# Kernel optimization log

Measured on AMD Instinct MI355X. Metric: run time of the kernel, lower is better.

## Reference

```python
import jax, jax.numpy as jnp
import numpy as np

B, C, H, W = 8, 128, 128, 128
HEADS = 4
EPS_LN = 1e-6
EPS_NORM = 1e-12


def layernorm2d(x, w, b):
    # channel-wise LN over axis 1 of (B,C,H,W)
    mean = x.mean(axis=1, keepdims=True)
    var = ((x - mean) ** 2).mean(axis=1, keepdims=True)
    xn = (x - mean) / jnp.sqrt(var + EPS_LN)
    return xn * w[None, :, None, None] + b[None, :, None, None]


def conv1x1(x, w):
    # w: (O, C) pointwise conv, no bias
    return jnp.einsum('bchw,oc->bohw', x, w)


def dwconv3x3(x, w):
    # w: (C, 1, 3, 3) depthwise conv, SAME padding, no bias
    return jax.lax.conv_general_dilated(
        x, w, window_strides=(1, 1), padding='SAME',
        dimension_numbers=('NCHW', 'OIHW', 'NCHW'),
        feature_group_count=x.shape[1])


def l2norm_lastdim(x):
    n = jnp.sqrt(jnp.sum(x * x, axis=-1, keepdims=True))
    return x / jnp.maximum(n, EPS_NORM)


def setup_inputs() -> dict:
    key = jax.random.key(0)
    ks = jax.random.split(key, 12)
    s = 0.05
    return {
        'state': jax.random.normal(ks[0], (B, C, H, W), jnp.float32),
        'dark': jax.random.normal(ks[1], (B, C, H, W), jnp.float32),
        'nq_w': jnp.ones((C,), jnp.float32),
        'nq_b': jnp.zeros((C,), jnp.float32),
        'nkv_w': jnp.ones((C,), jnp.float32),
        'nkv_b': jnp.zeros((C,), jnp.float32),
        'q_pw': jax.random.normal(ks[2], (C, C), jnp.float32) * s,
        'q_dw': jax.random.normal(ks[3], (C, 1, 3, 3), jnp.float32) * s,
        'k_pw': jax.random.normal(ks[4], (C, C), jnp.float32) * s,
        'k_dw': jax.random.normal(ks[5], (C, 1, 3, 3), jnp.float32) * s,
        'v_pw': jax.random.normal(ks[6], (C, C), jnp.float32) * s,
        'v_dw': jax.random.normal(ks[7], (C, 1, 3, 3), jnp.float32) * s,
        'proj_w': jax.random.normal(ks[8], (C, C), jnp.float32) * s,
        'temperature': jnp.ones((HEADS, 1, 1), jnp.float32),
    }


def reference(state, dark, nq_w, nq_b, nkv_w, nkv_b, q_pw, q_dw, k_pw, k_dw,
              v_pw, v_dw, proj_w, temperature):
    b, c, h, w = state.shape
    dc = c // HEADS
    residual = state

    q = dwconv3x3(conv1x1(layernorm2d(state, nq_w, nq_b), q_pw), q_dw)
    k = dwconv3x3(conv1x1(layernorm2d(dark, nkv_w, nkv_b), k_pw), k_dw)
    v = dwconv3x3(conv1x1(dark, v_pw), v_dw)

    q = q.reshape(b, HEADS, dc, h * w)
    k = k.reshape(b, HEADS, dc, h * w)
    v = v.reshape(b, HEADS, dc, h * w)

    q = l2norm_lastdim(q)
    k = l2norm_lastdim(k)

    # channel-wise attention map: (b, heads, dc, dc)
    attn = jnp.einsum('bhcd,bhed->bhce', q, k) * temperature[None]
    attn = jax.nn.softmax(attn, axis=-1)

    out = jnp.einsum('bhce,bhed->bhcd', attn, v).reshape(b, c, h, w)
    return conv1x1(out, proj_w) + residual
```

## Files before the change

### kernel.cpp

```cpp
#include <hip/hip_runtime.h>
#include <hip/hip_bf16.h>
#include <cstdint>

#define BB 8
#define CC 128
#define HH 128
#define WWID 128
#define HW (HH * WWID)
#define NHEADS 4
#define DC (CC / NHEADS)

typedef unsigned short u16x8 __attribute__((ext_vector_type(8)));
typedef unsigned short u16x4 __attribute__((ext_vector_type(4)));
typedef short s16x8 __attribute__((ext_vector_type(8)));
typedef float f32x4 __attribute__((ext_vector_type(4)));

__device__ __forceinline__ float bf2f(unsigned short u) {
  union { unsigned int i; float f; } c;
  c.i = ((unsigned int)u) << 16;
  return c.f;
}
__device__ __forceinline__ unsigned short f2bf(float f) {
  __hip_bfloat16 h = __float2bfloat16(f);
  return *reinterpret_cast<unsigned short*>(&h);
}

__global__ __launch_bounds__(128) void prep_weights_kernel(
    const float* __restrict__ q_pw, const float* __restrict__ k_pw,
    const float* __restrict__ v_pw, const float* __restrict__ proj_w,
    const float* __restrict__ nq_w, const float* __restrict__ nq_b,
    const float* __restrict__ nkv_w, const float* __restrict__ nkv_b,
    unsigned short* __restrict__ Wq, unsigned short* __restrict__ Wkv,
    unsigned short* __restrict__ Wproj, float* __restrict__ S1q,
    float* __restrict__ S2q, float* __restrict__ S1k, float* __restrict__ S2k) {
  int o = threadIdx.x;
  int which = blockIdx.x;
  if (which == 0) {
    float s1 = 0.f, s2 = 0.f;
    for (int c = 0; c < CC; ++c) {
      float w = q_pw[o * CC + c];
      float wl = w * nq_w[c];
      s1 += wl;
      s2 += w * nq_b[c];
      Wq[o * CC + c] = f2bf(wl);
    }
    S1q[o] = s1;
    S2q[o] = s2;
  } else if (which == 1) {
    float s1 = 0.f, s2 = 0.f;
    for (int c = 0; c < CC; ++c) {
      float w = k_pw[o * CC + c];
      float wl = w * nkv_w[c];
      s1 += wl;
      s2 += w * nkv_b[c];
      Wkv[o * CC + c] = f2bf(wl);
    }
    S1k[o] = s1;
    S2k[o] = s2;
  } else if (which == 2) {
    for (int c = 0; c < CC; ++c) Wkv[(128 + o) * CC + c] = f2bf(v_pw[o * CC + c]);
  } else {
    for (int c = 0; c < CC; ++c) Wproj[o * CC + c] = f2bf(proj_w[o * CC + c]);
  }
}

template <int MT, int LN_ROWS, int IN_BF16, int OUT_F32, int DO_RES>
__global__ __launch_bounds__(256) void conv_mfma_kernel(
    const void* __restrict__ Xv, const unsigned short* __restrict__ Wbf,
    const float* __restrict__ S1, const float* __restrict__ S2,
    const float* __restrict__ res, unsigned short* __restrict__ Out0,
    unsigned short* __restrict__ Out1, float* __restrict__ OutF) {
  constexpr int MPW = MT / 4;
  __shared__ unsigned short Xs[64 * 128];
  __shared__ float sstat[2][4][64];

  int tid = threadIdx.x;
  int lane = tid & 63, wid = tid >> 6;
  int p = tid & 63, qd = tid >> 6;
  int b = blockIdx.y;
  int p0 = blockIdx.x * 64;

  size_t xpix = (size_t)b * CC * HW + p0 + p;
  float s = 0.f, ss = 0.f;
#pragma unroll
  for (int chunk = 0; chunk < 4; ++chunk) {
    u16x8 vals;
#pragma unroll
    for (int j = 0; j < 8; ++j) {
      int c = chunk * 32 + qd * 8 + j;
      float x;
      if (IN_BF16) {
        unsigned short raw = ((const unsigned short*)Xv)[xpix + (size_t)c * HW];
        x = bf2f(raw);
        vals[j] = raw;
      } else {
        x = ((const float*)Xv)[xpix + (size_t)c * HW];
        vals[j] = f2bf(x);
      }
      if (LN_ROWS > 0) {
        s += x;
        ss += x * x;
      }
    }
    int colb = (chunk * 64 + qd * 16) ^ ((p & 7) << 4);
    *(u16x8*)((char*)Xs + p * 256 + colb) = vals;
  }
  if (LN_ROWS > 0) {
    sstat[0][qd][p] = s;
    sstat[1][qd][p] = ss;
  }
  __syncthreads();

  f32x4 acc[MPW][4];
#pragma unroll
  for (int mi = 0; mi < MPW; ++mi)
#pragma unroll
    for (int n = 0; n < 4; ++n) acc[mi][n] = (f32x4){0.f, 0.f, 0.f, 0.f};

#pragma unroll
  for (int kk = 0; kk < 4; ++kk) {
    s16x8 af[MPW], bfr[4];
#pragma unroll
    for (int mi = 0; mi < MPW; ++mi) {
      int o = wid * (MPW * 16) + mi * 16 + (lane & 15);
      af[mi] = *(const s16x8*)(Wbf + (size_t)o * CC + kk * 32 + (lane >> 4) * 8);
    }
#pragma unroll
    for (int n = 0; n < 4; ++n) {
      int pp = n * 16 + (lane & 15);
      int colb = (kk * 64 + (lane >> 4) * 16) ^ ((pp & 7) << 4);
      bfr[n] = *(s16x8*)((char*)Xs + pp * 256 + colb);
    }
#pragma unroll
    for (int mi = 0; mi < MPW; ++mi)
#pragma unroll
      for (int n = 0; n < 4; ++n)
        acc[mi][n] =
            __builtin_amdgcn_mfma_f32_16x16x32_bf16(af[mi], bfr[n], acc[mi][n], 0, 0, 0);
  }

#pragma unroll
  for (int n = 0; n < 4; ++n) {
    int pp = n * 16 + (lane & 15);
    float mu = 0.f, rr = 0.f;
    if (LN_ROWS > 0) {
      float t1 = sstat[0][0][pp] + sstat[0][1][pp] + sstat[0][2][pp] + sstat[0][3][pp];
      float t2 = sstat[1][0][pp] + sstat[1][1][pp] + sstat[1][2][pp] + sstat[1][3][pp];
      mu = t1 * (1.f / 128.f);
      float var = t2 * (1.f / 128.f) - mu * mu;
      rr = rsqrtf(var + 1e-6f);
    }
#pragma unroll
    for (int mi = 0; mi < MPW; ++mi) {
      int o_base = wid * (MPW * 16) + mi * 16;
      int oo = o_base + (lane >> 4) * 4;
      bool ln = (LN_ROWS > 0) && (o_base < LN_ROWS);
      float s1a[4] = {0.f, 0.f, 0.f, 0.f}, s2a[4] = {0.f, 0.f, 0.f, 0.f};
      if (ln) {
        float4 s1v = *(const float4*)(S1 + oo);
        float4 s2v = *(const float4*)(S2 + oo);
        s1a[0] = s1v.x; s1a[1] = s1v.y; s1a[2] = s1v.z; s1a[3] = s1v.w;
        s2a[0] = s2v.x; s2a[1] = s2v.y; s2a[2] = s2v.z; s2a[3] = s2v.w;
      }
#pragma unroll
      for (int r = 0; r < 4; ++r) {
        float v = acc[mi][n][r];
        if (ln) v = rr * (v - mu * s1a[r]) + s2a[r];
        int orow = oo + r;
        if (OUT_F32) {
          size_t off = ((size_t)b * CC + orow) * HW + p0 + pp;
          float q = v;
          if (DO_RES) q += res[off];
          OutF[off] = q;
        } else {
          unsigned short* dst = Out0;
          int od = orow;
          if (MT == 16 && orow >= 128) {
            dst = Out1;
            od = orow - 128;
          }
          dst[((size_t)b * CC + od) * HW + p0 + pp] = f2bf(v);
        }
      }
    }
  }
}

__global__ __launch_bounds__(256) void dwconv_kernel(
    const unsigned short* __restrict__ X, const float* __restrict__ Wd,
    unsigned short* __restrict__ Out) {
  __shared__ float plane[HW];
  int bc = blockIdx.x;
  int c = bc & (CC - 1);
  const unsigned short* src = X + (size_t)bc * HW;
  int tid = threadIdx.x;
#pragma unroll
  for (int i = 0; i < 8; ++i) {
    int idx8 = i * 256 + tid;
    u16x8 v = *(const u16x8*)(src + idx8 * 8);
    float4 f0 = {bf2f(v[0]), bf2f(v[1]), bf2f(v[2]), bf2f(v[3])};
    float4 f1 = {bf2f(v[4]), bf2f(v[5]), bf2f(v[6]), bf2f(v[7])};
    *(float4*)&plane[idx8 * 8] = f0;
    *(float4*)&plane[idx8 * 8 + 4] = f1;
  }
  float w[9];
#pragma unroll
  for (int j = 0; j < 9; ++j) w[j] = Wd[c * 9 + j];
  __syncthreads();

  unsigned short* dst = Out + (size_t)bc * HW;
  for (int i = 0; i < 16; ++i) {
    int pix4 = i * 1024 + tid * 4;
    int y = pix4 >> 7, x0 = pix4 & 127;
    float sacc[4];
    if (y > 0 && y < HH - 1 && x0 >= 4 && x0 <= 120) {
      const float* pc = &plane[y * WWID + x0];
#pragma unroll
      for (int dx = 0; dx < 4; ++dx) {
        sacc[dx] = w[0] * pc[dx - WWID - 1] + w[1] * pc[dx - WWID] + w[2] * pc[dx - WWID + 1] +
                   w[3] * pc[dx - 1] + w[4] * pc[dx] + w[5] * pc[dx + 1] +
                   w[6] * pc[dx + WWID - 1] + w[7] * pc[dx + WWID] + w[8] * pc[dx + WWID + 1];
      }
    } else {
#pragma unroll
      for (int dx = 0; dx < 4; ++dx) {
        int x = x0 + dx;
        float a = 0.f;
        for (int dy2 = -1; dy2 <= 1; ++dy2)
          for (int dx2 = -1; dx2 <= 1; ++dx2) {
            int yy = y + dy2, xx = x + dx2;
            if (yy >= 0 && yy < HH && xx >= 0 && xx < WWID)
              a += w[(dy2 + 1) * 3 + dx2 + 1] * plane[yy * WWID + xx];
          }
        sacc[dx] = a;
      }
    }
    u16x4 o;
#pragma unroll
    for (int dx = 0; dx < 4; ++dx) o[dx] = f2bf(sacc[dx]);
    *(u16x4*)(dst + pix4) = o;
  }
}

__global__ __launch_bounds__(256) void rownorm_kernel(
    const unsigned short* __restrict__ Q, const unsigned short* __restrict__ K,
    float* __restrict__ rq, float* __restrict__ rk) {
  int row = blockIdx.x;
  const unsigned short* src = blockIdx.y ? K : Q;
  float* dst = blockIdx.y ? rk : rq;
  const unsigned short* base = src + (size_t)row * HW;
  int tid = threadIdx.x;
  float ss = 0.f;
#pragma unroll
  for (int i = 0; i < 8; ++i) {
    u16x8 v = *(const u16x8*)(base + (i * 256 + tid) * 8);
#pragma unroll
    for (int j = 0; j < 8; ++j) {
      float f = bf2f(v[j]);
      ss += f * f;
    }
  }
#pragma unroll
  for (int m = 32; m >= 1; m >>= 1) ss += __shfl_xor(ss, m, 64);
  __shared__ float sred[4];
  if ((tid & 63) == 0) sred[tid >> 6] = ss;
  __syncthreads();
  if (tid == 0) {
    float t = sred[0] + sred[1] + sred[2] + sred[3];
    dst[row] = 1.f / fmaxf(sqrtf(t), 1e-12f);
  }
}

__global__ __launch_bounds__(256) void qk_partial_kernel(
    const unsigned short* __restrict__ Q, const unsigned short* __restrict__ K,
    float* __restrict__ part) {
  __shared__ float qs[32][129];
  __shared__ float ks[32][129];
  int ksid = blockIdx.x;
  int bh = blockIdx.y;
  int b = bh >> 2, h = bh & 3;
  size_t base = ((size_t)b * CC + h * DC) * HW + ksid * 512;
  int tid = threadIdx.x;
  int ci0 = (tid >> 4) * 2, ce0 = (tid & 15) * 2;
  float a00 = 0, a01 = 0, a10 = 0, a11 = 0;
  for (int ch = 0; ch < 4; ++ch) {
#pragma unroll
    for (int i = 0; i < 2; ++i) {
      int idx = i * 256 + tid;
      int r = idx >> 4, c8 = (idx & 15) * 8;
      u16x8 qv = *(const u16x8*)(Q + base + (size_t)r * HW + ch * 128 + c8);
      u16x8 kv = *(const u16x8*)(K + base + (size_t)r * HW + ch * 128 + c8);
#pragma unroll
      for (int j = 0; j < 8; ++j) {
        qs[r][c8 + j] = bf2f(qv[j]);
        ks[r][c8 + j] = bf2f(kv[j]);
      }
    }
    __syncthreads();
    for (int p = 0; p < 128; ++p) {
      float q0 = qs[ci0][p], q1 = qs[ci0 + 1][p];
      float k0 = ks[ce0][p], k1 = ks[ce0 + 1][p];
      a00 += q0 * k0;
      a01 += q0 * k1;
      a10 += q1 * k0;
      a11 += q1 * k1;
    }
    __syncthreads();
  }
  float* o = part + ((size_t)bh * 32 + ksid) * 1024;
  o[ci0 * 32 + ce0] = a00;
  o[ci0 * 32 + ce0 + 1] = a01;
  o[(ci0 + 1) * 32 + ce0] = a10;
  o[(ci0 + 1) * 32 + ce0 + 1] = a11;
}

__global__ __launch_bounds__(1024) void softmax_kernel(
    const float* __restrict__ part, const float* __restrict__ rq,
    const float* __restrict__ rk, const float* __restrict__ temp,
    float* __restrict__ attn) {
  int bh = blockIdx.x;
  int b = bh >> 2, h = bh & 3;
  int tid = threadIdx.x;
  int c = tid >> 5, e = tid & 31;
  const float* p0 = part + (size_t)bh * 32 * 1024 + tid;
  float s = 0.f;
#pragma unroll
  for (int ks = 0; ks < 32; ++ks) s += p0[(size_t)ks * 1024];
  s *= temp[h] * rq[b * CC + h * DC + c] * rk[b * CC + h * DC + e];
  float m = s;
#pragma unroll
  for (int w2 = 16; w2 >= 1; w2 >>= 1) m = fmaxf(m, __shfl_xor(m, w2, 64));
  float pe = __expf(s - m);
  float sum = pe;
#pragma unroll
  for (int w2 = 16; w2 >= 1; w2 >>= 1) sum += __shfl_xor(sum, w2, 64);
  attn[(size_t)bh * 1024 + tid] = pe / sum;
}

__global__ __launch_bounds__(256) void av_kernel(
    const float* __restrict__ attn, const unsigned short* __restrict__ V,
    unsigned short* __restrict__ Out) {
  __shared__ float vs[32][260];
  __shared__ float as[32][32];
  int pt = blockIdx.x, bh = blockIdx.y;
  int b = bh >> 2, h = bh & 3;
  size_t vbase = ((size_t)b * CC + h * DC) * HW + pt * 256;
  int tid = threadIdx.x;
#pragma unroll
  for (int i = 0; i < 4; ++i) {
    int idx = i * 256 + tid;
    int r = idx >> 5, c8 = (idx & 31) * 8;
    u16x8 vv = *(const u16x8*)(V + vbase + (size_t)r * HW + c8);
#pragma unroll
    for (int j = 0; j < 8; ++j) vs[r][c8 + j] = bf2f(vv[j]);
  }
#pragma unroll
  for (int i = 0; i < 4; ++i)
    ((float*)as)[i * 256 + tid] = attn[(size_t)bh * 1024 + i * 256 + tid];
  __syncthreads();

  int cg = tid >> 6;
  int p4 = (tid & 63) * 4;
  float4 acc[8];
#pragma unroll
  for (int ci = 0; ci < 8; ++ci) acc[ci] = make_float4(0.f, 0.f, 0.f, 0.f);
  for (int e = 0; e < 32; ++e) {
    float4 v4 = *(float4*)&vs[e][p4];
#pragma unroll
    for (int ci = 0; ci < 8; ++ci) {
      float a = as[cg * 8 + ci][e];
      acc[ci].x += a * v4.x;
      acc[ci].y += a * v4.y;
      acc[ci].z += a * v4.z;
      acc[ci].w += a * v4.w;
    }
  }
#pragma unroll
  for (int ci = 0; ci < 8; ++ci) {
    size_t off = ((size_t)b * CC + h * DC + cg * 8 + ci) * HW + pt * 256 + p4;
    u16x4 o;
    o[0] = f2bf(acc[ci].x);
    o[1] = f2bf(acc[ci].y);
    o[2] = f2bf(acc[ci].z);
    o[3] = f2bf(acc[ci].w);
    *(u16x4*)(Out + off) = o;
  }
}

extern "C" void kernel_launch(void* const* d_in, const int* in_sizes, int n_in,
                              void* d_out, int out_size, void* d_ws, size_t ws_size,
                              hipStream_t stream) {
  (void)in_sizes; (void)n_in; (void)out_size; (void)ws_size;
  const float* state = (const float*)d_in[0];
  const float* dark = (const float*)d_in[1];
  const float* nq_w = (const float*)d_in[2];
  const float* nq_b = (const float*)d_in[3];
  const float* nkv_w = (const float*)d_in[4];
  const float* nkv_b = (const float*)d_in[5];
  const float* q_pw = (const float*)d_in[6];
  const float* q_dw = (const float*)d_in[7];
  const float* k_pw = (const float*)d_in[8];
  const float* k_dw = (const float*)d_in[9];
  const float* v_pw = (const float*)d_in[10];
  const float* v_dw = (const float*)d_in[11];
  const float* proj_w = (const float*)d_in[12];
  const float* temp = (const float*)d_in[13];
  float* out = (float*)d_out;

  char* ws = (char*)d_ws;
  const size_t REG = 32ull << 20;
  unsigned short* R0 = (unsigned short*)(ws + 0 * REG);
  unsigned short* R1 = (unsigned short*)(ws + 1 * REG);
  unsigned short* R2 = (unsigned short*)(ws + 2 * REG);
  unsigned short* R3 = (unsigned short*)(ws + 3 * REG);
  char* sm = ws + 4 * REG;
  float* part = (float*)sm; sm += (size_t)32 * 32 * 1024 * 4;
  float* attn = (float*)sm; sm += (size_t)32 * 1024 * 4;
  float* rq = (float*)sm; sm += BB * CC * 4;
  float* rk = (float*)sm; sm += BB * CC * 4;
  unsigned short* Wq = (unsigned short*)sm; sm += (size_t)CC * CC * 2;
  unsigned short* Wkv = (unsigned short*)sm; sm += (size_t)2 * CC * CC * 2;
  unsigned short* Wproj = (unsigned short*)sm; sm += (size_t)CC * CC * 2;
  float* S1q = (float*)sm; sm += CC * 4;
  float* S2q = (float*)sm; sm += CC * 4;
  float* S1k = (float*)sm; sm += CC * 4;
  float* S2k = (float*)sm; sm += CC * 4;

  prep_weights_kernel<<<dim3(4), 128, 0, stream>>>(
      q_pw, k_pw, v_pw, proj_w, nq_w, nq_b, nkv_w, nkv_b, Wq, Wkv, Wproj, S1q,
      S2q, S1k, S2k);

  dim3 cgrid(HW / 64, BB);
  conv_mfma_kernel<8, 128, 0, 0, 0><<<cgrid, 256, 0, stream>>>(
      state, Wq, S1q, S2q, nullptr, R0, nullptr, nullptr);
  dwconv_kernel<<<dim3(BB * CC), 256, 0, stream>>>(R0, q_dw, R1);

  conv_mfma_kernel<16, 128, 0, 0, 0><<<cgrid, 256, 0, stream>>>(
      dark, Wkv, S1k, S2k, nullptr, R2, R3, nullptr);
  dwconv_kernel<<<dim3(BB * CC), 256, 0, stream>>>(R2, k_dw, R0);
  dwconv_kernel<<<dim3(BB * CC), 256, 0, stream>>>(R3, v_dw, R2);

  rownorm_kernel<<<dim3(BB * CC, 2), 256, 0, stream>>>(R1, R0, rq, rk);

  qk_partial_kernel<<<dim3(32, BB * NHEADS), 256, 0, stream>>>(R1, R0, part);
  softmax_kernel<<<dim3(BB * NHEADS), 1024, 0, stream>>>(part, rq, rk, temp, attn);

  av_kernel<<<dim3(HW / 256, BB * NHEADS), 256, 0, stream>>>(attn, R2, R3);

  conv_mfma_kernel<8, 0, 1, 1, 1><<<cgrid, 256, 0, stream>>>(
      R3, Wproj, nullptr, nullptr, state, nullptr, nullptr, out);
}
```

Before: 572.7 us.

## Vectorize conv load/store via quad transposes, strip dwconv, fuse row norms

The pointwise-conv kernel now loads and stores four contiguous pixels per thread (float4/u16x4) and uses lane-shuffle quad transposes to move between the pixel-major and channel-major layouts. LayerNorm statistics are computed once into shared memory instead of per output. The depthwise conv is split into four row strips per plane, giving more blocks and less LDS per block. The squared-norm reduction is fused into the q/k dwconv with atomicAdd, which removes the separate rownorm pass but needs a memset and makes the summation order nondeterministic.

```diff
diff --git a/kernel.cpp b/kernel.cpp
--- a/kernel.cpp
+++ b/kernel.cpp
@@ -23,6 +23,16 @@
 __device__ __forceinline__ unsigned short f2bf(float f) {
   __hip_bfloat16 h = __float2bfloat16(f);
   return *reinterpret_cast<unsigned short*>(&h);
+}
+
+__device__ __forceinline__ void quad_transpose(float& v0, float& v1, float& v2,
+                                               float& v3, int r) {
+  float u0 = __shfl_xor(v0, 1), u1 = __shfl_xor(v1, 1);
+  float u2 = __shfl_xor(v2, 1), u3 = __shfl_xor(v3, 1);
+  if ((r & 1) == 0) { v1 = u0; v3 = u2; } else { v0 = u1; v2 = u3; }
+  u0 = __shfl_xor(v0, 2); u1 = __shfl_xor(v1, 2);
+  u2 = __shfl_xor(v2, 2); u3 = __shfl_xor(v3, 2);
+  if ((r & 2) == 0) { v2 = u0; v3 = u1; } else { v0 = u2; v1 = u3; }
 }
 
 __global__ __launch_bounds__(128) void prep_weights_kernel(
@@ -73,43 +83,54 @@
   constexpr int MPW = MT / 4;
   __shared__ unsigned short Xs[64 * 128];
   __shared__ float sstat[2][4][64];
+  __shared__ float muA[64], rrA[64];
 
   int tid = threadIdx.x;
   int lane = tid & 63, wid = tid >> 6;
-  int p = tid & 63, qd = tid >> 6;
   int b = blockIdx.y;
   int p0 = blockIdx.x * 64;
 
-  size_t xpix = (size_t)b * CC * HW + p0 + p;
+  int r = tid & 3;
+  int pg = (tid >> 2) & 15;
   float s = 0.f, ss = 0.f;
-#pragma unroll
-  for (int chunk = 0; chunk < 4; ++chunk) {
-    u16x8 vals;
-#pragma unroll
-    for (int j = 0; j < 8; ++j) {
-      int c = chunk * 32 + qd * 8 + j;
-      float x;
-      if (IN_BF16) {
-        unsigned short raw = ((const unsigned short*)Xv)[xpix + (size_t)c * HW];
-        x = bf2f(raw);
-        vals[j] = raw;
-      } else {
-        x = ((const float*)Xv)[xpix + (size_t)c * HW];
-        vals[j] = f2bf(x);
-      }
-      if (LN_ROWS > 0) {
-        s += x;
-        ss += x * x;
-      }
-    }
-    int colb = (chunk * 64 + qd * 16) ^ ((p & 7) << 4);
-    *(u16x8*)((char*)Xs + p * 256 + colb) = vals;
+  size_t xbase = (size_t)b * CC * HW + p0 + pg * 4;
+#pragma unroll
+  for (int i = 0; i < 8; ++i) {
+    int cb = i * 16 + wid * 4;
+    int ch = cb + r;
+    float v0, v1, v2, v3;
+    if (IN_BF16) {
+      u16x4 u = *(const u16x4*)((const unsigned short*)Xv + xbase + (size_t)ch * HW);
+      v0 = bf2f(u[0]); v1 = bf2f(u[1]); v2 = bf2f(u[2]); v3 = bf2f(u[3]);
+    } else {
+      float4 f = *(const float4*)((const float*)Xv + xbase + (size_t)ch * HW);
+      v0 = f.x; v1 = f.y; v2 = f.z; v3 = f.w;
+    }
+    quad_transpose(v0, v1, v2, v3, r);
+    if (LN_ROWS > 0) {
+      s += v0 + v1 + v2 + v3;
+      ss += v0 * v0 + v1 * v1 + v2 * v2 + v3 * v3;
+    }
+    int p = pg * 4 + r;
+    u16x4 o;
+    o[0] = f2bf(v0); o[1] = f2bf(v1); o[2] = f2bf(v2); o[3] = f2bf(v3);
+    *(u16x4*)((char*)Xs + p * 256 + ((cb * 2) ^ ((p & 7) << 4))) = o;
   }
   if (LN_ROWS > 0) {
-    sstat[0][qd][p] = s;
-    sstat[1][qd][p] = ss;
+    int p = pg * 4 + r;
+    sstat[0][wid][p] = s;
+    sstat[1][wid][p] = ss;
   }
   __syncthreads();
+
+  if (LN_ROWS > 0 && wid == 0) {
+    float t1 = sstat[0][0][lane] + sstat[0][1][lane] + sstat[0][2][lane] + sstat[0][3][lane];
+    float t2 = sstat[1][0][lane] + sstat[1][1][lane] + sstat[1][2][lane] + sstat[1][3][lane];
+    float mu = t1 * (1.f / 128.f);
+    float var = t2 * (1.f / 128.f) - mu * mu;
+    muA[lane] = mu;
+    rrA[lane] = rsqrtf(var + 1e-6f);
+  }
 
   f32x4 acc[MPW][4];
 #pragma unroll
@@ -139,135 +160,120 @@
             __builtin_amdgcn_mfma_f32_16x16x32_bf16(af[mi], bfr[n], acc[mi][n], 0, 0, 0);
   }
 
-#pragma unroll
-  for (int n = 0; n < 4; ++n) {
-    int pp = n * 16 + (lane & 15);
-    float mu = 0.f, rr = 0.f;
-    if (LN_ROWS > 0) {
-      float t1 = sstat[0][0][pp] + sstat[0][1][pp] + sstat[0][2][pp] + sstat[0][3][pp];
-      float t2 = sstat[1][0][pp] + sstat[1][1][pp] + sstat[1][2][pp] + sstat[1][3][pp];
-      mu = t1 * (1.f / 128.f);
-      float var = t2 * (1.f / 128.f) - mu * mu;
-      rr = rsqrtf(var + 1e-6f);
-    }
-#pragma unroll
-    for (int mi = 0; mi < MPW; ++mi) {
-      int o_base = wid * (MPW * 16) + mi * 16;
-      int oo = o_base + (lane >> 4) * 4;
-      bool ln = (LN_ROWS > 0) && (o_base < LN_ROWS);
-      float s1a[4] = {0.f, 0.f, 0.f, 0.f}, s2a[4] = {0.f, 0.f, 0.f, 0.f};
+  if (LN_ROWS > 0) __syncthreads();
+
+  int q = (lane >> 2) & 3, m = lane & 3, g = lane >> 4;
+#pragma unroll
+  for (int mi = 0; mi < MPW; ++mi) {
+    int o_base = wid * (MPW * 16) + mi * 16;
+    int o = o_base + g * 4 + m;
+    bool ln = (LN_ROWS > 0) && (o_base < LN_ROWS);
+    float s1v = 0.f, s2v = 0.f;
+    if (ln) { s1v = S1[o]; s2v = S2[o]; }
+#pragma unroll
+    for (int n = 0; n < 4; ++n) {
+      float v0 = acc[mi][n][0], v1 = acc[mi][n][1], v2 = acc[mi][n][2], v3 = acc[mi][n][3];
+      quad_transpose(v0, v1, v2, v3, m);
+      int px0 = n * 16 + q * 4;
       if (ln) {
-        float4 s1v = *(const float4*)(S1 + oo);
-        float4 s2v = *(const float4*)(S2 + oo);
-        s1a[0] = s1v.x; s1a[1] = s1v.y; s1a[2] = s1v.z; s1a[3] = s1v.w;
-        s2a[0] = s2v.x; s2a[1] = s2v.y; s2a[2] = s2v.z; s2a[3] = s2v.w;
+        float4 muv = *(float4*)&muA[px0];
+        float4 rrv = *(float4*)&rrA[px0];
+        v0 = rrv.x * (v0 - muv.x * s1v) + s2v;
+        v1 = rrv.y * (v1 - muv.y * s1v) + s2v;
+        v2 = rrv.z * (v2 - muv.z * s1v) + s2v;
+        v3 = rrv.w * (v3 - muv.w * s1v) + s2v;
       }
-#pragma unroll
-      for (int r = 0; r < 4; ++r) {
-        float v = acc[mi][n][r];
-        if (ln) v = rr * (v - mu * s1a[r]) + s2a[r];
-        int orow = oo + r;
-        if (OUT_F32) {
-          size_t off = ((size_t)b * CC + orow) * HW + p0 + pp;
-          float q = v;
-          if (DO_RES) q += res[off];
-          OutF[off] = q;
-        } else {
-          unsigned short* dst = Out0;
-          int od = orow;
-          if (MT == 16 && orow >= 128) {
-            dst = Out1;
-            od = orow - 128;
-          }
-          dst[((size_t)b * CC + od) * HW + p0 + pp] = f2bf(v);
+      if (OUT_F32) {
+        size_t off = ((size_t)b * CC + o) * HW + p0 + px0;
+        if (DO_RES) {
+          float4 rv = *(const float4*)(res + off);
+          v0 += rv.x; v1 += rv.y; v2 += rv.z; v3 += rv.w;
         }
+        float4 ov = {v0, v1, v2, v3};
+        *(float4*)(OutF + off) = ov;
+      } else {
+        unsigned short* dst = Out0;
+        int od = o;
+        if (MT == 16 && o >= 128) { dst = Out1; od = o - 128; }
+        u16x4 ov;
+        ov[0] = f2bf(v0); ov[1] = f2bf(v1); ov[2] = f2bf(v2); ov[3] = f2bf(v3);
+        *(u16x4*)(dst + ((size_t)b * CC + od) * HW + p0 + px0) = ov;
       }
     }
   }
 }
 
+template <int NORM>
 __global__ __launch_bounds__(256) void dwconv_kernel(
     const unsigned short* __restrict__ X, const float* __restrict__ Wd,
-    unsigned short* __restrict__ Out) {
-  __shared__ float plane[HW];
-  int bc = blockIdx.x;
+    unsigned short* __restrict__ Out, float* __restrict__ normOut) {
+  __shared__ float plane[34 * 128];
+  int strip = blockIdx.x & 3;
+  int bc = blockIdx.x >> 2;
   int c = bc & (CC - 1);
+  int y0 = strip * 32;
   const unsigned short* src = X + (size_t)bc * HW;
   int tid = threadIdx.x;
-#pragma unroll
-  for (int i = 0; i < 8; ++i) {
-    int idx8 = i * 256 + tid;
-    u16x8 v = *(const u16x8*)(src + idx8 * 8);
-    float4 f0 = {bf2f(v[0]), bf2f(v[1]), bf2f(v[2]), bf2f(v[3])};
-    float4 f1 = {bf2f(v[4]), bf2f(v[5]), bf2f(v[6]), bf2f(v[7])};
-    *(float4*)&plane[idx8 * 8] = f0;
-    *(float4*)&plane[idx8 * 8 + 4] = f1;
+
+  for (int idx = tid; idx < 34 * 16; idx += 256) {
+    int row = idx >> 4;
+    int x8 = (idx & 15) * 8;
+    int y = y0 - 1 + row;
+    float4 f0 = {0, 0, 0, 0}, f1 = {0, 0, 0, 0};
+    if (y >= 0 && y < HH) {
+      u16x8 v = *(const u16x8*)(src + (size_t)y * WWID + x8);
+      f0 = make_float4(bf2f(v[0]), bf2f(v[1]), bf2f(v[2]), bf2f(v[3]));
+      f1 = make_float4(bf2f(v[4]), bf2f(v[5]), bf2f(v[6]), bf2f(v[7]));
+    }
+    *(float4*)&plane[row * 128 + x8] = f0;
+    *(float4*)&plane[row * 128 + x8 + 4] = f1;
   }
   float w[9];
 #pragma unroll
   for (int j = 0; j < 9; ++j) w[j] = Wd[c * 9 + j];
   __syncthreads();
 
-  unsigned short* dst = Out + (size_t)bc * HW;
-  for (int i = 0; i < 16; ++i) {
+  float ssq = 0.f;
+  unsigned short* dst = Out + (size_t)bc * HW + y0 * WWID;
+#pragma unroll
+  for (int i = 0; i < 4; ++i) {
     int pix4 = i * 1024 + tid * 4;
-    int y = pix4 >> 7, x0 = pix4 & 127;
-    float sacc[4];
-    if (y > 0 && y < HH - 1 && x0 >= 4 && x0 <= 120) {
-      const float* pc = &plane[y * WWID + x0];
-#pragma unroll
-      for (int dx = 0; dx < 4; ++dx) {
-        sacc[dx] = w[0] * pc[dx - WWID - 1] + w[1] * pc[dx - WWID] + w[2] * pc[dx - WWID + 1] +
-                   w[3] * pc[dx - 1] + w[4] * pc[dx] + w[5] * pc[dx + 1] +
-                   w[6] * pc[dx + WWID - 1] + w[7] * pc[dx + WWID] + w[8] * pc[dx + WWID + 1];
-      }
+    int ly = pix4 >> 7, x0 = pix4 & 127;
+    const float* pc = &plane[(ly + 1) * 128 + x0];
+    float sv[4];
+    if (x0 >= 4 && x0 <= 120) {
+#pragma unroll
+      for (int dx = 0; dx < 4; ++dx)
+        sv[dx] = w[0] * pc[dx - 129] + w[1] * pc[dx - 128] + w[2] * pc[dx - 127] +
+                 w[3] * pc[dx - 1] + w[4] * pc[dx] + w[5] * pc[dx + 1] +
+                 w[6] * pc[dx + 127] + w[7] * pc[dx + 128] + w[8] * pc[dx + 129];
     } else {
 #pragma unroll
       for (int dx = 0; dx < 4; ++dx) {
         int x = x0 + dx;
         float a = 0.f;
-        for (int dy2 = -1; dy2 <= 1; ++dy2)
+        for (int dy = -1; dy <= 1; ++dy)
           for (int dx2 = -1; dx2 <= 1; ++dx2) {
-            int yy = y + dy2, xx = x + dx2;
-            if (yy >= 0 && yy < HH && xx >= 0 && xx < WWID)
-              a += w[(dy2 + 1) * 3 + dx2 + 1] * plane[yy * WWID + xx];
+            int xx = x + dx2;
+            if (xx >= 0 && xx < WWID)
+              a += w[(dy + 1) * 3 + dx2 + 1] * plane[(ly + 1 + dy) * 128 + xx];
           }
-        sacc[dx] = a;
+        sv[dx] = a;
       }
     }
+    if (NORM) ssq += sv[0] * sv[0] + sv[1] * sv[1] + sv[2] * sv[2] + sv[3] * sv[3];
     u16x4 o;
 #pragma unroll
-    for (int dx = 0; dx < 4; ++dx) o[dx] = f2bf(sacc[dx]);
+    for (int dx = 0; dx < 4; ++dx) o[dx] = f2bf(sv[dx]);
     *(u16x4*)(dst + pix4) = o;
   }
-}
-
-__global__ __launch_bounds__(256) void rownorm_kernel(
-    const unsigned short* __restrict__ Q, const unsigned short* __restrict__ K,
-    float* __restrict__ rq, float* __restrict__ rk) {
-  int row = blockIdx.x;
-  const unsigned short* src = blockIdx.y ? K : Q;
-  float* dst = blockIdx.y ? rk : rq;
-  const unsigned short* base = src + (size_t)row * HW;
-  int tid = threadIdx.x;
-  float ss = 0.f;
-#pragma unroll
-  for (int i = 0; i < 8; ++i) {
-    u16x8 v = *(const u16x8*)(base + (i * 256 + tid) * 8);
-#pragma unroll
-    for (int j = 0; j < 8; ++j) {
-      float f = bf2f(v[j]);
-      ss += f * f;
-    }
-  }
-#pragma unroll
-  for (int m = 32; m >= 1; m >>= 1) ss += __shfl_xor(ss, m, 64);
-  __shared__ float sred[4];
-  if ((tid & 63) == 0) sred[tid >> 6] = ss;
-  __syncthreads();
-  if (tid == 0) {
-    float t = sred[0] + sred[1] + sred[2] + sred[3];
-    dst[row] = 1.f / fmaxf(sqrtf(t), 1e-12f);
+  if (NORM) {
+#pragma unroll
+    for (int m2 = 32; m2 >= 1; m2 >>= 1) ssq += __shfl_xor(ssq, m2, 64);
+    __shared__ float sred[4];
+    if ((tid & 63) == 0) sred[tid >> 6] = ssq;
+    __syncthreads();
+    if (tid == 0) atomicAdd(&normOut[bc], sred[0] + sred[1] + sred[2] + sred[3]);
   }
 }
 
@@ -287,13 +293,13 @@
 #pragma unroll
     for (int i = 0; i < 2; ++i) {
       int idx = i * 256 + tid;
-      int r = idx >> 4, c8 = (idx & 15) * 8;
-      u16x8 qv = *(const u16x8*)(Q + base + (size_t)r * HW + ch * 128 + c8);
-      u16x8 kv = *(const u16x8*)(K + base + (size_t)r * HW + ch * 128 + c8);
+      int rr = idx >> 4, c8 = (idx & 15) * 8;
+      u16x8 qv = *(const u16x8*)(Q + base + (size_t)rr * HW + ch * 128 + c8);
+      u16x8 kv = *(const u16x8*)(K + base + (size_t)rr * HW + ch * 128 + c8);
 #pragma unroll
       for (int j = 0; j < 8; ++j) {
-        qs[r][c8 + j] = bf2f(qv[j]);
-        ks[r][c8 + j] = bf2f(kv[j]);
+        qs[rr][c8 + j] = bf2f(qv[j]);
+        ks[rr][c8 + j] = bf2f(kv[j]);
       }
     }
     __syncthreads();
@@ -326,7 +332,9 @@
   float s = 0.f;
 #pragma unroll
   for (int ks = 0; ks < 32; ++ks) s += p0[(size_t)ks * 1024];
-  s *= temp[h] * rq[b * CC + h * DC + c] * rk[b * CC + h * DC + e];
+  float nq = sqrtf(rq[b * CC + h * DC + c]);
+  float nk = sqrtf(rk[b * CC + h * DC + e]);
+  s *= temp[h] / (fmaxf(nq, 1e-12f) * fmaxf(nk, 1e-12f));
   float m = s;
 #pragma unroll
   for (int w2 = 16; w2 >= 1; w2 >>= 1) m = fmaxf(m, __shfl_xor(m, w2, 64));
@@ -349,10 +357,10 @@
 #pragma unroll
   for (int i = 0; i < 4; ++i) {
     int idx = i * 256 + tid;
-    int r = idx >> 5, c8 = (idx & 31) * 8;
-    u16x8 vv = *(const u16x8*)(V + vbase + (size_t)r * HW + c8);
-#pragma unroll
-    for (int j = 0; j < 8; ++j) vs[r][c8 + j] = bf2f(vv[j]);
+    int rr = idx >> 5, c8 = (idx & 31) * 8;
+    u16x8 vv = *(const u16x8*)(V + vbase + (size_t)rr * HW + c8);
+#pragma unroll
+    for (int j = 0; j < 8; ++j) vs[rr][c8 + j] = bf2f(vv[j]);
   }
 #pragma unroll
   for (int i = 0; i < 4; ++i)
@@ -426,6 +434,8 @@
   float* S1k = (float*)sm; sm += CC * 4;
   float* S2k = (float*)sm; sm += CC * 4;
 
+  hipMemsetAsync(rq, 0, 2 * BB * CC * sizeof(float), stream);
+
   prep_weights_kernel<<<dim3(4), 128, 0, stream>>>(
       q_pw, k_pw, v_pw, proj_w, nq_w, nq_b, nkv_w, nkv_b, Wq, Wkv, Wproj, S1q,
       S2q, S1k, S2k);
@@ -433,14 +443,12 @@
   dim3 cgrid(HW / 64, BB);
   conv_mfma_kernel<8, 128, 0, 0, 0><<<cgrid, 256, 0, stream>>>(
       state, Wq, S1q, S2q, nullptr, R0, nullptr, nullptr);
-  dwconv_kernel<<<dim3(BB * CC), 256, 0, stream>>>(R0, q_dw, R1);
+  dwconv_kernel<1><<<dim3(BB * CC * 4), 256, 0, stream>>>(R0, q_dw, R1, rq);
 
   conv_mfma_kernel<16, 128, 0, 0, 0><<<cgrid, 256, 0, stream>>>(
       dark, Wkv, S1k, S2k, nullptr, R2, R3, nullptr);
-  dwconv_kernel<<<dim3(BB * CC), 256, 0, stream>>>(R2, k_dw, R0);
-  dwconv_kernel<<<dim3(BB * CC), 256, 0, stream>>>(R3, v_dw, R2);
-
-  rownorm_kernel<<<dim3(BB * CC, 2), 256, 0, stream>>>(R1, R0, rq, rk);
+  dwconv_kernel<1><<<dim3(BB * CC * 4), 256, 0, stream>>>(R2, k_dw, R0, rk);
+  dwconv_kernel<0><<<dim3(BB * CC * 4), 256, 0, stream>>>(R3, v_dw, R2, nullptr);
 
   qk_partial_kernel<<<dim3(32, BB * NHEADS), 256, 0, stream>>>(R1, R0, part);
   softmax_kernel<<<dim3(BB * NHEADS), 1024, 0, stream>>>(part, rq, rk, temp, attn);
```

Result: faster. 468.2 us (-18.3%).
